# Kernel optimization log

Measured on AMD Instinct MI355X. Metric: run time of the kernel, lower is better.

Reference implementation:

```python
import jax, jax.numpy as jnp
import numpy as np

IN_DIM = 256      # in_dim
OUT_DIM = 4608    # out_dim = 6*768 (adaLN projection)
M = 68            # ceil(sqrt(max(in_dim, out_dim)))
PAD = M * M       # 4624 padded (perfect-square) dim
B = 16384         # token batch
INIT_SCALE = 0.02


def setup_inputs() -> dict:
    key = jax.random.key(0)
    k1, k2, k3 = jax.random.split(key, 3)
    x = jax.random.normal(k1, (B, IN_DIM), dtype=jnp.float32)
    # Monarch block-diagonal factors: M blocks of M x M each, scaled per init_scale
    L = jax.random.normal(k2, (M, M, M), dtype=jnp.float32) * INIT_SCALE
    R = jax.random.normal(k3, (M, M, M), dtype=jnp.float32) * INIT_SCALE
    bias = jnp.zeros((OUT_DIM,), dtype=jnp.float32)
    return {"x": x, "L": L, "R": R, "bias": bias}


def _monarch_linear(x, L, R, bias):
    # zero-pad input up to the perfect-square dim n = M*M
    b = x.shape[0]
    xp = jnp.pad(x, ((0, 0), (0, PAD - IN_DIM)))          # [B, PAD]
    x2 = xp.reshape(b, M, M)                               # [B, k=M, p=M]
    # first block-diagonal matmul: per-block x @ L[k]^T
    t1 = jnp.einsum('bkp,kqp->bkq', x2, L)                 # [B, k, q]
    # Monarch inner permutation (block transpose)
    t1 = jnp.swapaxes(t1, 1, 2)                            # [B, l=q, r=k]
    # second block-diagonal matmul
    t2 = jnp.einsum('blr,lsr->bls', t1, R)                 # [B, l, s]
    y = jnp.swapaxes(t2, 1, 2).reshape(b, PAD)             # [B, PAD] (s-major)
    # slice to out_dim, add bias
    return y[:, :OUT_DIM] + bias


def reference(x, L, R, bias):
    return _monarch_linear(x, L, R, bias)
```

## Files before the change

### kernel.cpp

```cpp
#include <hip/hip_runtime.h>


typedef float f4 __attribute__((ext_vector_type(4)));
typedef short s8v __attribute__((ext_vector_type(8)));

namespace {
constexpr int MM    = 68;
constexpr int IN_D  = 256;
constexpr int OUT_D = 4608;
constexpr int NTH   = 256;
constexpr int BM    = 32;
constexpr int EPW   = 36;
}

__device__ __forceinline__ unsigned short f2bf(float f) {
  unsigned int u = __float_as_uint(f);
  u += 0x7FFFu + ((u >> 16) & 1u);
  return (unsigned short)(u >> 16);
}

__global__ __launch_bounds__(NTH, 1)
void pack_w2(const float* __restrict__ L, const float* __restrict__ R,
             unsigned short* __restrict__ Wpk)
{
  const int g    = blockIdx.x * 4 + (threadIdx.x >> 6);
  const int lane = threadIdx.x & 63;
  const int jc   = g >> 3;
  const int ks   = g & 7;
  const int j    = jc * 16 + (lane & 15);
  const int s    = j / MM;
  const int l    = j - s * MM;
  const int k0   = ks * 32 + (lane >> 4) * 8;
  unsigned int h[4];
#pragma unroll
  for (int i2 = 0; i2 < 4; ++i2) {
    unsigned int w2[2];
#pragma unroll
    for (int e = 0; e < 2; ++e) {
      int k = k0 + i2 * 2 + e;
      int r = k / MM, p = k - r * MM;
      float w = L[(r * MM + l) * MM + p] * R[(l * MM + s) * MM + r];
      w2[e] = f2bf(w);
    }
    h[i2] = w2[0] | (w2[1] << 16);
  }
  uint4 v; v.x = h[0]; v.y = h[1]; v.z = h[2]; v.w = h[3];
  *(uint4*)(Wpk + ((size_t)g * 64 + lane) * 8) = v;
}

__global__ __launch_bounds__(NTH, 3)
void mono_gemm2(const float* __restrict__ x, const unsigned short* __restrict__ Wpk,
                const float* __restrict__ bias, float* __restrict__ out)
{
  __shared__ float ep[4][BM][EPW];
  const int tid  = threadIdx.x;
  const int lane = tid & 63;
  const int wv   = tid >> 6;
  const int lrow = lane & 15;
  const int lgrp = lane >> 4;
  const int tile = blockIdx.x >> 1;
  const int jh   = blockIdx.x & 1;
  const long tb  = (long)tile * BM;

  s8v afr[2][8];
#pragma unroll
  for (int mt = 0; mt < 2; ++mt) {
#pragma unroll
    for (int ks = 0; ks < 8; ++ks) {
      const float* xp = x + (tb + mt * 16 + lrow) * IN_D + ks * 32 + lgrp * 8;
      f4 a = *(const f4*)(xp);
      f4 b = *(const f4*)(xp + 4);
      s8v t;
      t[0] = (short)f2bf(a.x); t[1] = (short)f2bf(a.y);
      t[2] = (short)f2bf(a.z); t[3] = (short)f2bf(a.w);
      t[4] = (short)f2bf(b.x); t[5] = (short)f2bf(b.y);
      t[6] = (short)f2bf(b.z); t[7] = (short)f2bf(b.w);
      afr[mt][ks] = t;
    }
  }

  float (*eps)[EPW] = ep[wv];

#pragma unroll 1
  for (int i = 0; i < 18; ++i) {
    const int j0 = ((i * 4 + wv) << 5) + jh * 2304;
#pragma unroll
    for (int c = 0; c < 2; ++c) {
      const int jcIdx = (j0 >> 4) + c;
      uint4 bfr[8];
#pragma unroll
      for (int ks = 0; ks < 8; ++ks)
        bfr[ks] = *(const uint4*)(Wpk + (((size_t)jcIdx * 8 + ks) * 64 + lane) * 8);
      f4 a0 = {0.f, 0.f, 0.f, 0.f}, a1 = {0.f, 0.f, 0.f, 0.f};
#pragma unroll
      for (int ks = 0; ks < 8; ++ks) {
        s8v bf = *(s8v*)&bfr[ks];
        a0 = __builtin_amdgcn_mfma_f32_16x16x32_bf16(afr[0][ks], bf, a0, 0, 0, 0);
        a1 = __builtin_amdgcn_mfma_f32_16x16x32_bf16(afr[1][ks], bf, a1, 0, 0, 0);
      }
#pragma unroll
      for (int q = 0; q < 4; ++q) {
        eps[lgrp * 4 + q][c * 16 + lrow]      = a0[q];
        eps[16 + lgrp * 4 + q][c * 16 + lrow] = a1[q];
      }
    }
    const f4 bv = *(const f4*)(bias + j0 + (lane & 7) * 4);
#pragma unroll
    for (int sw = 0; sw < 4; ++sw) {
      const int rr = sw * 8 + (lane >> 3);
      f4 v = *(const f4*)(&eps[rr][(lane & 7) * 4]);
      f4 o;
      o.x = v.x + bv.x; o.y = v.y + bv.y; o.z = v.z + bv.z; o.w = v.w + bv.w;
      *(f4*)(out + (tb + rr) * OUT_D + j0 + (lane & 7) * 4) = o;
    }
  }
}

namespace {
constexpr int TTF  = 16;
constexpr int XROW = IN_D + 4;
constexpr int TPAD = 4 * MM + 4;
}
template <int P4M>
__device__ __forceinline__ void phaseA_f(const float* xls, const float* Lrow0, float* t1w)
{
  float acc[17];
#pragma unroll
  for (int li = 0; li < 17; ++li) acc[li] = 0.f;
#pragma unroll 1
  for (int p4 = 0; p4 < P4M; ++p4) {
    f4 xv = *(const f4*)(xls + 4 * p4);
    f4 Lv[17];
#pragma unroll
    for (int li = 0; li < 17; ++li) Lv[li] = *(const f4*)(Lrow0 + (size_t)li * MM + 4 * p4);
#pragma unroll
    for (int li = 0; li < 17; ++li) {
      acc[li] = fmaf(xv.x, Lv[li].x, acc[li]); acc[li] = fmaf(xv.y, Lv[li].y, acc[li]);
      acc[li] = fmaf(xv.z, Lv[li].z, acc[li]); acc[li] = fmaf(xv.w, Lv[li].w, acc[li]);
    }
  }
#pragma unroll
  for (int li = 0; li < 17; ++li) t1w[li] = acc[li];
}
__global__ __launch_bounds__(NTH, 4)
void monarch_fused(const float* __restrict__ x, const float* __restrict__ L,
                   const float* __restrict__ R, const float* __restrict__ bias,
                   float* __restrict__ out)
{
  __shared__ float xs[TTF * XROW];
  __shared__ float t1s[TTF * TPAD];
  const int tid = threadIdx.x;
  const long tb = (long)blockIdx.x * TTF;
#pragma unroll
  for (int k = 0; k < (TTF * IN_D / 4) / NTH; ++k) {
    int i = k * NTH + tid; int tok = i >> 6; int pos = i & 63;
    *(f4*)(&xs[tok * XROW + 4 * pos]) = *(const f4*)(x + (tb + tok) * IN_D + 4 * pos);
  }
  __syncthreads();
  {
    const int tok = tid & 15; const int seg = tid >> 4;
    const int r = seg >> 2; const int lq = seg & 3;
    const float* xls = &xs[tok * XROW + r * MM];
    const float* Lrow0 = L + (size_t)(r * MM + lq * 17) * MM;
    float* t1w = &t1s[tok * TPAD + r * MM + lq * 17];
    if (r < 3) phaseA_f<17>(xls, Lrow0, t1w); else phaseA_f<13>(xls, Lrow0, t1w);
  }
  __syncthreads();
  {
    const int g = tid / 17; const int m = tid - g * 17; const int l4 = 4 * m;
#pragma unroll 1
    for (int j = 0; j < 5; ++j) {
      const int s = g + 15 * j;
      const bool act = (tid < 255) && (s < MM) && (s < MM - 1 || m < 13);
      const int scol = s * MM + l4;
      f4 R0, R1, R2, R3, bv;
      if (act) {
        R0 = *(const f4*)(R + (size_t)(l4 + 0) * (MM * MM) + (size_t)s * MM);
        R1 = *(const f4*)(R + (size_t)(l4 + 1) * (MM * MM) + (size_t)s * MM);
        R2 = *(const f4*)(R + (size_t)(l4 + 2) * (MM * MM) + (size_t)s * MM);
        R3 = *(const f4*)(R + (size_t)(l4 + 3) * (MM * MM) + (size_t)s * MM);
        bv = *(const f4*)(bias + scol);
      }
#pragma unroll 2
      for (int t = 0; t < TTF; ++t) {
        if (act) {
          const float* t1p = t1s + t * TPAD + l4;
          f4 a0 = *(const f4*)(t1p); f4 a1 = *(const f4*)(t1p + MM);
          f4 a2 = *(const f4*)(t1p + 2 * MM); f4 a3 = *(const f4*)(t1p + 3 * MM);
          f4 o;
          o.x = fmaf(a3.x, R0.w, fmaf(a2.x, R0.z, fmaf(a1.x, R0.y, fmaf(a0.x, R0.x, bv.x))));
          o.y = fmaf(a3.y, R1.w, fmaf(a2.y, R1.z, fmaf(a1.y, R1.y, fmaf(a0.y, R1.x, bv.y))));
          o.z = fmaf(a3.z, R2.w, fmaf(a2.z, R2.z, fmaf(a1.z, R2.y, fmaf(a0.z, R2.x, bv.z))));
          o.w = fmaf(a3.w, R3.w, fmaf(a2.w, R3.z, fmaf(a1.w, R3.y, fmaf(a0.w, R3.x, bv.w))));
          *(f4*)(out + (tb + t) * OUT_D + scol) = o;
        }
      }
    }
  }
}

extern "C" void kernel_launch(void* const* d_in, const int* in_sizes, int n_in,
                              void* d_out, int out_size, void* d_ws, size_t ws_size,
                              hipStream_t stream) {
  const float* x    = (const float*)d_in[0];
  const float* L    = (const float*)d_in[1];
  const float* R    = (const float*)d_in[2];
  const float* bias = (const float*)d_in[3];
  float* out = (float*)d_out;

  const int ntok = in_sizes[0] / IN_D;
  const size_t wb_bytes = (size_t)OUT_D * IN_D * sizeof(unsigned short);

  if (ws_size >= wb_bytes) {
    unsigned short* Wpk = (unsigned short*)d_ws;
    pack_w2<<<576, NTH, 0, stream>>>(L, R, Wpk);
    mono_gemm2<<<(ntok / BM) * 2, NTH, 0, stream>>>(x, Wpk, bias, out);
  } else {
    monarch_fused<<<ntok / TTF, NTH, 0, stream>>>(x, L, R, bias, out);
  }
}
```

Before: 111.0 us.

## Enlarge token tile to 64 rows and stream one 16-col weight tile per wave

Each block now handles 64 tokens across all output columns instead of 32 tokens across half the columns. Every loaded weight fragment therefore feeds four MFMA row tiles instead of two, which halves the weight reads per token and drops the duplicated x load and bf16 conversion between column halves. The trade-offs are more registers for A fragments (launch bounds change from 3 blocks per CU to 1), only 256 blocks, and narrower 16-column output stores.

```diff
diff --git a/kernel.cpp b/kernel.cpp
--- a/kernel.cpp
+++ b/kernel.cpp
@@ -9,8 +9,9 @@
 constexpr int IN_D  = 256;
 constexpr int OUT_D = 4608;
 constexpr int NTH   = 256;
-constexpr int BM    = 32;
-constexpr int EPW   = 36;
+constexpr int BM    = 64;
+constexpr int EPW   = 20;
+constexpr int NJT   = OUT_D / 16;
 }
 
 __device__ __forceinline__ unsigned short f2bf(float f) {
@@ -48,8 +49,8 @@
   *(uint4*)(Wpk + ((size_t)g * 64 + lane) * 8) = v;
 }
 
-__global__ __launch_bounds__(NTH, 3)
-void mono_gemm2(const float* __restrict__ x, const unsigned short* __restrict__ Wpk,
+__global__ __launch_bounds__(NTH, 1)
+void mono_gemm3(const float* __restrict__ x, const unsigned short* __restrict__ Wpk,
                 const float* __restrict__ bias, float* __restrict__ out)
 {
   __shared__ float ep[4][BM][EPW];
@@ -58,13 +59,11 @@
   const int wv   = tid >> 6;
   const int lrow = lane & 15;
   const int lgrp = lane >> 4;
-  const int tile = blockIdx.x >> 1;
-  const int jh   = blockIdx.x & 1;
-  const long tb  = (long)tile * BM;
-
-  s8v afr[2][8];
-#pragma unroll
-  for (int mt = 0; mt < 2; ++mt) {
+  const long tb  = (long)blockIdx.x * BM;
+
+  s8v afr[4][8];
+#pragma unroll
+  for (int mt = 0; mt < 4; ++mt) {
 #pragma unroll
     for (int ks = 0; ks < 8; ++ks) {
       const float* xp = x + (tb + mt * 16 + lrow) * IN_D + ks * 32 + lgrp * 8;
@@ -82,36 +81,37 @@
   float (*eps)[EPW] = ep[wv];
 
 #pragma unroll 1
-  for (int i = 0; i < 18; ++i) {
-    const int j0 = ((i * 4 + wv) << 5) + jh * 2304;
-#pragma unroll
-    for (int c = 0; c < 2; ++c) {
-      const int jcIdx = (j0 >> 4) + c;
-      uint4 bfr[8];
-#pragma unroll
-      for (int ks = 0; ks < 8; ++ks)
-        bfr[ks] = *(const uint4*)(Wpk + (((size_t)jcIdx * 8 + ks) * 64 + lane) * 8);
-      f4 a0 = {0.f, 0.f, 0.f, 0.f}, a1 = {0.f, 0.f, 0.f, 0.f};
-#pragma unroll
-      for (int ks = 0; ks < 8; ++ks) {
-        s8v bf = *(s8v*)&bfr[ks];
-        a0 = __builtin_amdgcn_mfma_f32_16x16x32_bf16(afr[0][ks], bf, a0, 0, 0, 0);
-        a1 = __builtin_amdgcn_mfma_f32_16x16x32_bf16(afr[1][ks], bf, a1, 0, 0, 0);
-      }
-#pragma unroll
-      for (int q = 0; q < 4; ++q) {
-        eps[lgrp * 4 + q][c * 16 + lrow]      = a0[q];
-        eps[16 + lgrp * 4 + q][c * 16 + lrow] = a1[q];
-      }
-    }
-    const f4 bv = *(const f4*)(bias + j0 + (lane & 7) * 4);
+  for (int t = wv; t < NJT; t += 4) {
+    const int j0 = t * 16;
+    uint4 bfr[8];
+#pragma unroll
+    for (int ks = 0; ks < 8; ++ks)
+      bfr[ks] = *(const uint4*)(Wpk + (((size_t)t * 8 + ks) * 64 + lane) * 8);
+    f4 acc0 = {0.f,0.f,0.f,0.f}, acc1 = {0.f,0.f,0.f,0.f};
+    f4 acc2 = {0.f,0.f,0.f,0.f}, acc3 = {0.f,0.f,0.f,0.f};
+#pragma unroll
+    for (int ks = 0; ks < 8; ++ks) {
+      s8v bf = *(s8v*)&bfr[ks];
+      acc0 = __builtin_amdgcn_mfma_f32_16x16x32_bf16(afr[0][ks], bf, acc0, 0, 0, 0);
+      acc1 = __builtin_amdgcn_mfma_f32_16x16x32_bf16(afr[1][ks], bf, acc1, 0, 0, 0);
+      acc2 = __builtin_amdgcn_mfma_f32_16x16x32_bf16(afr[2][ks], bf, acc2, 0, 0, 0);
+      acc3 = __builtin_amdgcn_mfma_f32_16x16x32_bf16(afr[3][ks], bf, acc3, 0, 0, 0);
+    }
+#pragma unroll
+    for (int q = 0; q < 4; ++q) {
+      eps[ 0 + lgrp * 4 + q][lrow] = acc0[q];
+      eps[16 + lgrp * 4 + q][lrow] = acc1[q];
+      eps[32 + lgrp * 4 + q][lrow] = acc2[q];
+      eps[48 + lgrp * 4 + q][lrow] = acc3[q];
+    }
+    const f4 bv = *(const f4*)(bias + j0 + (lane & 3) * 4);
 #pragma unroll
     for (int sw = 0; sw < 4; ++sw) {
-      const int rr = sw * 8 + (lane >> 3);
-      f4 v = *(const f4*)(&eps[rr][(lane & 7) * 4]);
+      const int rr = sw * 16 + (lane >> 2);
+      f4 v = *(const f4*)(&eps[rr][(lane & 3) * 4]);
       f4 o;
       o.x = v.x + bv.x; o.y = v.y + bv.y; o.z = v.z + bv.z; o.w = v.w + bv.w;
-      *(f4*)(out + (tb + rr) * OUT_D + j0 + (lane & 7) * 4) = o;
+      *(f4*)(out + (tb + rr) * OUT_D + j0 + (lane & 3) * 4) = o;
     }
   }
 }
@@ -214,7 +214,7 @@
   if (ws_size >= wb_bytes) {
     unsigned short* Wpk = (unsigned short*)d_ws;
     pack_w2<<<576, NTH, 0, stream>>>(L, R, Wpk);
-    mono_gemm2<<<(ntok / BM) * 2, NTH, 0, stream>>>(x, Wpk, bias, out);
+    mono_gemm3<<<ntok / BM, NTH, 0, stream>>>(x, Wpk, bias, out);
   } else {
     monarch_fused<<<ntok / TTF, NTH, 0, stream>>>(x, L, R, bias, out);
   }
```

Measured after the change: 135.3 us. 1.22x slower.
